# Kernel tuning notes

Hardware: AMD Instinct MI355X
Metric: run time of the kernel (lower is better)

Reference implementation:

```python
import jax, jax.numpy as jnp
import numpy as np

NUM_JOINTS = 21
BN_EPS = 1e-5


def hand_adjacency():
    J = NUM_JOINTS
    a = np.zeros((J, J), dtype=np.float32)
    # wrist to finger bases
    for j in (1, 5, 9, 13, 17):
        a[0, j] = a[j, 0] = 1
    # finger chains
    for base in (1, 5, 9, 13, 17):
        for i in range(base, base + 3):
            a[i, i + 1] = a[i + 1, i] = 1
    a += np.eye(J, dtype=np.float32)
    d = a.sum(axis=1)
    dinv = np.power(d, -0.5)
    dinv[np.isinf(dinv)] = 0.0
    D = np.diag(dinv)
    return (D @ a @ D).astype(np.float32)


def setup_inputs() -> dict:
    key = jax.random.key(0)
    ks = jax.random.split(key, 16)
    S, B, HD = 256, 128, 42
    IN, HID = 2, 64
    x = jax.random.normal(ks[0], (S, B, HD), dtype=jnp.float32)
    # xavier-uniform weights
    lim1 = float(np.sqrt(6.0 / (IN + HID)))
    lim2 = float(np.sqrt(6.0 / (HID + IN)))
    W1 = jax.random.uniform(ks[1], (IN, HID), minval=-lim1, maxval=lim1, dtype=jnp.float32)
    b1 = jnp.zeros((HID,), dtype=jnp.float32)
    W2 = jax.random.uniform(ks[2], (HID, IN), minval=-lim2, maxval=lim2, dtype=jnp.float32)
    b2 = jnp.zeros((IN,), dtype=jnp.float32)
    # BatchNorm (eval mode): affine params + running stats
    g1 = 1.0 + 0.1 * jax.random.normal(ks[3], (HID,), dtype=jnp.float32)
    be1 = 0.1 * jax.random.normal(ks[4], (HID,), dtype=jnp.float32)
    m1 = 0.1 * jax.random.normal(ks[5], (HID,), dtype=jnp.float32)
    v1 = 0.5 + jax.random.uniform(ks[6], (HID,), dtype=jnp.float32)
    g2 = 1.0 + 0.1 * jax.random.normal(ks[7], (IN,), dtype=jnp.float32)
    be2 = 0.1 * jax.random.normal(ks[8], (IN,), dtype=jnp.float32)
    m2 = 0.1 * jax.random.normal(ks[9], (IN,), dtype=jnp.float32)
    v2 = 0.5 + jax.random.uniform(ks[10], (IN,), dtype=jnp.float32)
    adj = jnp.asarray(hand_adjacency())
    return {"x": x, "adj": adj, "W1": W1, "b1": b1, "W2": W2, "b2": b2,
            "g1": g1, "be1": be1, "m1": m1, "v1": v1,
            "g2": g2, "be2": be2, "m2": m2, "v2": v2}


def _gcn_bn(h, adj, W, b, g, be, m, v, act):
    # h: (S, B, J, Cin) -> (S, B, J, Cout)
    s = jnp.einsum('sbjc,cd->sbjd', h, W)          # feature transform
    o = jnp.einsum('ij,sbjd->sbid', adj, s) + b    # joint aggregation + bias
    o = (o - m) * (g * jax.lax.rsqrt(v + BN_EPS)) + be  # BN eval, per-channel
    return jax.nn.relu(o) if act else o


def reference(x, adj, W1, b1, W2, b2, g1, be1, m1, v1, g2, be2, m2, v2):
    S, B, HD = x.shape
    C = HD // NUM_JOINTS
    h = x.reshape(S, B, NUM_JOINTS, C)
    h = _gcn_bn(h, adj, W1, b1, g1, be1, m1, v1, act=True)   # dropout is identity in eval
    h = _gcn_bn(h, adj, W2, b2, g2, be2, m2, v2, act=False)
    return h.reshape(S, B, HD) + x
```

## Files before the change

### kernel.cpp

```cpp
#include <hip/hip_runtime.h>

typedef float f2 __attribute__((ext_vector_type(2)));

#define NJ 21

#define W00 0.16666667f
#define W0B 0.23570226f
#define W33 0.33333333f
#define WMT 0.40824829f
#define WTT 0.5f

template<int PAT>
__device__ __forceinline__ float dpp_add(float v) {
    int r = __builtin_amdgcn_update_dpp(0, __float_as_int(v), PAT, 0xF, 0xF, true);
    return v + __int_as_float(r);
}

__device__ __forceinline__ void aggregate(const f2* __restrict__ s, f2* __restrict__ d) {
    d[0] = W00 * s[0] + W0B * (s[1] + s[5] + s[9] + s[13] + s[17]);
#pragma unroll
    for (int f = 1; f <= 17; f += 4) {
        d[f]     = W0B * s[0] + W33 * (s[f] + s[f + 1]);
        d[f + 1] = W33 * (s[f] + s[f + 1] + s[f + 2]);
        d[f + 2] = W33 * (s[f + 1] + s[f + 2]) + WMT * s[f + 3];
        d[f + 3] = WMT * s[f + 2] + WTT * s[f + 3];
    }
}

__global__ __launch_bounds__(256) void hgcn_kernel(
    const float* __restrict__ x,
    const float* __restrict__ adj,
    const float* __restrict__ W1,
    const float* __restrict__ b1,
    const float* __restrict__ W2,
    const float* __restrict__ b2,
    const float* __restrict__ g1,
    const float* __restrict__ be1,
    const float* __restrict__ m1,
    const float* __restrict__ v1,
    const float* __restrict__ g2,
    const float* __restrict__ be2,
    const float* __restrict__ m2,
    const float* __restrict__ v2,
    float* __restrict__ out)
{
    (void)adj;
    __shared__ float4 sc1[67];
    __shared__ float  sc2[64];
    __shared__ float  sD[2];
    __shared__ float  xs[64 * 42];
    __shared__ float  os[64 * 42];

    const int tid = threadIdx.x;

    const float4* __restrict__ xg =
        (const float4*)(x + (size_t)blockIdx.x * (64 * 42));
    float4* xs4 = (float4*)xs;
    const float4 r0 = xg[tid];
    const float4 r1 = xg[tid + 256];
    float4 r2;
    if (tid < 160) r2 = xg[tid + 512];

    if (tid < 64) {
        const int d = tid;
        const float k1  = g1[d] * rsqrtf(v1[d] + 1e-5f);
        const float A   = W1[d]      * k1;
        const float B   = W1[64 + d] * k1;
        const float C   = (b1[d] - m1[d]) * k1 + be1[d];
        const float k20 = g2[0] * rsqrtf(v2[0] + 1e-5f);
        const float k21 = g2[1] * rsqrtf(v2[1] + 1e-5f);
        sc1[d + (d >> 4)] = make_float4(A, B, C, W2[2 * d] * k20);
        sc2[d] = W2[2 * d + 1] * k21;
        if (d < 2) {
            const float k2 = (d == 0) ? k20 : k21;
            sD[d] = (b2[d] - m2[d]) * k2 + be2[d];
        }
    }

    xs4[tid]       = r0;
    xs4[tid + 256] = r1;
    if (tid < 160) xs4[tid + 512] = r2;
    __syncthreads();

    const int tl = tid >> 2;
    const int q  = tid & 3;

    const float2* __restrict__ xt = (const float2*)(xs + tl * 42);
    f2 h[NJ];
#pragma unroll
    for (int j = 0; j < NJ; ++j) {
        const float2 v = xt[j];
        h[j] = (f2){v.x, v.y};
    }

    f2 a[NJ + 1];
    aggregate(h, a);
    a[NJ] = (f2){0.f, 0.f};

    f2 ap0[11], ap1[11];
#pragma unroll
    for (int k = 0; k < 11; ++k) {
        ap0[k] = (f2){a[2 * k].x, a[2 * k + 1].x};
        ap1[k] = (f2){a[2 * k].y, a[2 * k + 1].y};
    }

    f2 s0[11], s1[11];
#pragma unroll
    for (int k = 0; k < 11; ++k) { s0[k] = (f2){0.f, 0.f}; s1[k] = (f2){0.f, 0.f}; }

    const int cbase = q * 17;
#pragma unroll
    for (int dd = 0; dd < 16; ++dd) {
        const float4 c  = sc1[cbase + dd];
        const float w21 = sc2[(q << 4) + dd];
#pragma unroll
        for (int k = 0; k < 11; ++k) {
            f2 v = ap0[k] * c.x + ap1[k] * c.y + c.z;
            v = __builtin_elementwise_max(v, (f2){0.f, 0.f});
            s0[k] += v * c.w;
            s1[k] += v * w21;
        }
    }

#pragma unroll
    for (int k = 0; k < 11; ++k) {
        s0[k].x = dpp_add<0xB1>(s0[k].x);  s0[k].x = dpp_add<0x4E>(s0[k].x);
        s0[k].y = dpp_add<0xB1>(s0[k].y);  s0[k].y = dpp_add<0x4E>(s0[k].y);
        s1[k].x = dpp_add<0xB1>(s1[k].x);  s1[k].x = dpp_add<0x4E>(s1[k].x);
        s1[k].y = dpp_add<0xB1>(s1[k].y);  s1[k].y = dpp_add<0x4E>(s1[k].y);
    }

    f2 vv[NJ], o[NJ];
#pragma unroll
    for (int j = 0; j < NJ; ++j) {
        vv[j].x = (j & 1) ? s0[j >> 1].y : s0[j >> 1].x;
        vv[j].y = (j & 1) ? s1[j >> 1].y : s1[j >> 1].x;
    }
    aggregate(vv, o);

    const int lo = (q == 0) ? 0 : (q == 1) ? 5 : (q == 2) ? 11 : 16;
    const int hi = (q == 0) ? 5 : (q == 1) ? 11 : (q == 2) ? 16 : 21;
    float2* __restrict__ ot = (float2*)(os + tl * 42);
#pragma unroll
    for (int i = 0; i < NJ; ++i) {
        if (i >= lo && i < hi) {
            float2 st; st.x = o[i].x; st.y = o[i].y;
            ot[i] = st;
        }
    }
    __syncthreads();

    const float4 Df = make_float4(sD[0], sD[1], sD[0], sD[1]);
    float4* __restrict__ og = (float4*)(out + (size_t)blockIdx.x * (64 * 42));
    const float4* os4 = (const float4*)os;

    float4 o0 = os4[tid],       x0 = xs4[tid];
    float4 o1 = os4[tid + 256], x1 = xs4[tid + 256];
    og[tid] = make_float4(o0.x + x0.x + Df.x, o0.y + x0.y + Df.y,
                          o0.z + x0.z + Df.z, o0.w + x0.w + Df.w);
    og[tid + 256] = make_float4(o1.x + x1.x + Df.x, o1.y + x1.y + Df.y,
                                o1.z + x1.z + Df.z, o1.w + x1.w + Df.w);
    if (tid < 160) {
        float4 o2 = os4[tid + 512], x2 = xs4[tid + 512];
        og[tid + 512] = make_float4(o2.x + x2.x + Df.x, o2.y + x2.y + Df.y,
                                    o2.z + x2.z + Df.z, o2.w + x2.w + Df.w);
    }
}

extern "C" void kernel_launch(void* const* d_in, const int* in_sizes, int n_in,
                              void* d_out, int out_size, void* d_ws, size_t ws_size,
                              hipStream_t stream) {
    (void)in_sizes; (void)n_in; (void)d_ws; (void)ws_size; (void)out_size;
    const float* x   = (const float*)d_in[0];
    const float* adj = (const float*)d_in[1];
    const float* W1  = (const float*)d_in[2];
    const float* b1  = (const float*)d_in[3];
    const float* W2  = (const float*)d_in[4];
    const float* b2  = (const float*)d_in[5];
    const float* g1  = (const float*)d_in[6];
    const float* be1 = (const float*)d_in[7];
    const float* m1  = (const float*)d_in[8];
    const float* v1  = (const float*)d_in[9];
    const float* g2  = (const float*)d_in[10];
    const float* be2 = (const float*)d_in[11];
    const float* m2  = (const float*)d_in[12];
    const float* v2  = (const float*)d_in[13];

    hgcn_kernel<<<512, 256, 0, stream>>>(x, adj, W1, b1, W2, b2,
                                         g1, be1, m1, v1, g2, be2, m2, v2,
                                         (float*)d_out);
}
```

Measured before the change: 90.10 us.

## Make each wave self-contained with 8-lane channel split and wave barriers

Restructures the kernel so each wave processes its own 8 tokens with private LDS staging and per-wave constant tables, replacing block-wide __syncthreads with wave barriers. The hidden-channel loop is split across 8 lanes per token (8 channels each) instead of 4 lanes (16 channels), adding a ds_swizzle reduction step. The grid doubles to 1024 blocks to expose more parallelism and reduce per-thread serial work, at the cost of redundant per-wave constant setup and an extra cross-lane reduction.

```diff
diff --git a/kernel.cpp b/kernel.cpp
--- a/kernel.cpp
+++ b/kernel.cpp
@@ -16,6 +16,11 @@
     return v + __int_as_float(r);
 }
 
+__device__ __forceinline__ float swz4_add(float v) {
+    int r = __builtin_amdgcn_ds_swizzle(__float_as_int(v), 0x101F);
+    return v + __int_as_float(r);
+}
+
 __device__ __forceinline__ void aggregate(const f2* __restrict__ s, f2* __restrict__ d) {
     d[0] = W00 * s[0] + W0B * (s[1] + s[5] + s[9] + s[13] + s[17]);
 #pragma unroll
@@ -27,7 +32,7 @@
     }
 }
 
-__global__ __launch_bounds__(256) void hgcn_kernel(
+__global__ __launch_bounds__(256, 4) void hgcn_kernel(
     const float* __restrict__ x,
     const float* __restrict__ adj,
     const float* __restrict__ W1,
@@ -45,52 +50,53 @@
     float* __restrict__ out)
 {
     (void)adj;
-    __shared__ float4 sc1[67];
-    __shared__ float  sc2[64];
-    __shared__ float  sD[2];
-    __shared__ float  xs[64 * 42];
-    __shared__ float  os[64 * 42];
+    __shared__ float  xs[4][336];
+    __shared__ float  os[4][336];
+    __shared__ float4 sc1[4][68];
+    __shared__ float  sc2[4][68];
+    __shared__ float  sD[4][2];
 
     const int tid = threadIdx.x;
+    const int wv  = tid >> 6;
+    const int ln  = tid & 63;
 
     const float4* __restrict__ xg =
-        (const float4*)(x + (size_t)blockIdx.x * (64 * 42));
-    float4* xs4 = (float4*)xs;
-    const float4 r0 = xg[tid];
-    const float4 r1 = xg[tid + 256];
-    float4 r2;
-    if (tid < 160) r2 = xg[tid + 512];
-
-    if (tid < 64) {
-        const int d = tid;
-        const float k1  = g1[d] * rsqrtf(v1[d] + 1e-5f);
-        const float A   = W1[d]      * k1;
-        const float B   = W1[64 + d] * k1;
-        const float C   = (b1[d] - m1[d]) * k1 + be1[d];
+        (const float4*)(x + ((size_t)blockIdx.x * 32 + (size_t)wv * 8) * 42);
+    const float4 r0 = xg[ln];
+    float4 r1;
+    if (ln < 20) r1 = xg[64 + ln];
+
+    {
+        const int dch = ln;
+        const float k1  = g1[dch] * rsqrtf(v1[dch] + 1e-5f);
+        const float A   = W1[dch]      * k1;
+        const float B   = W1[64 + dch] * k1;
+        const float C   = (b1[dch] - m1[dch]) * k1 + be1[dch];
         const float k20 = g2[0] * rsqrtf(v2[0] + 1e-5f);
         const float k21 = g2[1] * rsqrtf(v2[1] + 1e-5f);
-        sc1[d + (d >> 4)] = make_float4(A, B, C, W2[2 * d] * k20);
-        sc2[d] = W2[2 * d + 1] * k21;
-        if (d < 2) {
-            const float k2 = (d == 0) ? k20 : k21;
-            sD[d] = (b2[d] - m2[d]) * k2 + be2[d];
+        const int   idx = dch + (dch >> 4);
+        sc1[wv][idx] = make_float4(A, B, C, W2[2 * dch] * k20);
+        sc2[wv][idx] = W2[2 * dch + 1] * k21;
+        if (dch < 2) {
+            const float k2 = (dch == 0) ? k20 : k21;
+            sD[wv][dch] = (b2[dch] - m2[dch]) * k2 + be2[dch];
         }
     }
 
-    xs4[tid]       = r0;
-    xs4[tid + 256] = r1;
-    if (tid < 160) xs4[tid + 512] = r2;
-    __syncthreads();
-
-    const int tl = tid >> 2;
-    const int q  = tid & 3;
-
-    const float2* __restrict__ xt = (const float2*)(xs + tl * 42);
+    float4* xs4 = (float4*)xs[wv];
+    xs4[ln] = r0;
+    if (ln < 20) xs4[64 + ln] = r1;
+    __builtin_amdgcn_wave_barrier();
+
+    const int tl = ln >> 3;
+    const int li = ln & 7;
+
+    const float2* __restrict__ xt = (const float2*)(xs[wv] + tl * 42);
     f2 h[NJ];
 #pragma unroll
     for (int j = 0; j < NJ; ++j) {
-        const float2 v = xt[j];
-        h[j] = (f2){v.x, v.y};
+        const float2 t = xt[j];
+        h[j] = (f2){t.x, t.y};
     }
 
     f2 a[NJ + 1];
@@ -108,11 +114,15 @@
 #pragma unroll
     for (int k = 0; k < 11; ++k) { s0[k] = (f2){0.f, 0.f}; s1[k] = (f2){0.f, 0.f}; }
 
-    const int cbase = q * 17;
-#pragma unroll
-    for (int dd = 0; dd < 16; ++dd) {
-        const float4 c  = sc1[cbase + dd];
-        const float w21 = sc2[(q << 4) + dd];
+    const float4* __restrict__ c1w = (const float4*)sc1[wv];
+    const float*  __restrict__ c2w = sc2[wv];
+    const int dbase = li * 8;
+#pragma unroll
+    for (int dd = 0; dd < 8; ++dd) {
+        const int   dg  = dbase + dd;
+        const int   idx = dg + (dg >> 4);
+        const float4 c  = c1w[idx];
+        const float w21 = c2w[idx];
 #pragma unroll
         for (int k = 0; k < 11; ++k) {
             f2 v = ap0[k] * c.x + ap1[k] * c.y + c.z;
@@ -124,10 +134,10 @@
 
 #pragma unroll
     for (int k = 0; k < 11; ++k) {
-        s0[k].x = dpp_add<0xB1>(s0[k].x);  s0[k].x = dpp_add<0x4E>(s0[k].x);
-        s0[k].y = dpp_add<0xB1>(s0[k].y);  s0[k].y = dpp_add<0x4E>(s0[k].y);
-        s1[k].x = dpp_add<0xB1>(s1[k].x);  s1[k].x = dpp_add<0x4E>(s1[k].x);
-        s1[k].y = dpp_add<0xB1>(s1[k].y);  s1[k].y = dpp_add<0x4E>(s1[k].y);
+        s0[k].x = dpp_add<0xB1>(s0[k].x); s0[k].x = dpp_add<0x4E>(s0[k].x); s0[k].x = swz4_add(s0[k].x);
+        s0[k].y = dpp_add<0xB1>(s0[k].y); s0[k].y = dpp_add<0x4E>(s0[k].y); s0[k].y = swz4_add(s0[k].y);
+        s1[k].x = dpp_add<0xB1>(s1[k].x); s1[k].x = dpp_add<0x4E>(s1[k].x); s1[k].x = swz4_add(s1[k].x);
+        s1[k].y = dpp_add<0xB1>(s1[k].y); s1[k].y = dpp_add<0x4E>(s1[k].y); s1[k].y = swz4_add(s1[k].y);
     }
 
     f2 vv[NJ], o[NJ];
@@ -138,32 +148,31 @@
     }
     aggregate(vv, o);
 
-    const int lo = (q == 0) ? 0 : (q == 1) ? 5 : (q == 2) ? 11 : 16;
-    const int hi = (q == 0) ? 5 : (q == 1) ? 11 : (q == 2) ? 16 : 21;
-    float2* __restrict__ ot = (float2*)(os + tl * 42);
-#pragma unroll
-    for (int i = 0; i < NJ; ++i) {
-        if (i >= lo && i < hi) {
-            float2 st; st.x = o[i].x; st.y = o[i].y;
-            ot[i] = st;
+    const int lo = (li * 21) >> 3;
+    const int hi = ((li + 1) * 21) >> 3;
+    float2* __restrict__ ot = (float2*)(os[wv] + tl * 42);
+#pragma unroll
+    for (int j = 0; j < NJ; ++j) {
+        if (j >= lo && j < hi) {
+            float2 st; st.x = o[j].x; st.y = o[j].y;
+            ot[j] = st;
         }
     }
-    __syncthreads();
-
-    const float4 Df = make_float4(sD[0], sD[1], sD[0], sD[1]);
-    float4* __restrict__ og = (float4*)(out + (size_t)blockIdx.x * (64 * 42));
-    const float4* os4 = (const float4*)os;
-
-    float4 o0 = os4[tid],       x0 = xs4[tid];
-    float4 o1 = os4[tid + 256], x1 = xs4[tid + 256];
-    og[tid] = make_float4(o0.x + x0.x + Df.x, o0.y + x0.y + Df.y,
-                          o0.z + x0.z + Df.z, o0.w + x0.w + Df.w);
-    og[tid + 256] = make_float4(o1.x + x1.x + Df.x, o1.y + x1.y + Df.y,
-                                o1.z + x1.z + Df.z, o1.w + x1.w + Df.w);
-    if (tid < 160) {
-        float4 o2 = os4[tid + 512], x2 = xs4[tid + 512];
-        og[tid + 512] = make_float4(o2.x + x2.x + Df.x, o2.y + x2.y + Df.y,
-                                    o2.z + x2.z + Df.z, o2.w + x2.w + Df.w);
+    __builtin_amdgcn_wave_barrier();
+
+    const float Df0 = sD[wv][0], Df1 = sD[wv][1];
+    const float4 Df = make_float4(Df0, Df1, Df0, Df1);
+    float4* __restrict__ og =
+        (float4*)(out + ((size_t)blockIdx.x * 32 + (size_t)wv * 8) * 42);
+    const float4* os4 = (const float4*)os[wv];
+
+    const float4 o0 = os4[ln], x0 = xs4[ln];
+    og[ln] = make_float4(o0.x + x0.x + Df.x, o0.y + x0.y + Df.y,
+                         o0.z + x0.z + Df.z, o0.w + x0.w + Df.w);
+    if (ln < 20) {
+        const float4 o1 = os4[64 + ln], x1 = xs4[64 + ln];
+        og[64 + ln] = make_float4(o1.x + x1.x + Df.x, o1.y + x1.y + Df.y,
+                                  o1.z + x1.z + Df.z, o1.w + x1.w + Df.w);
     }
 }
 
@@ -186,7 +195,7 @@
     const float* m2  = (const float*)d_in[12];
     const float* v2  = (const float*)d_in[13];
 
-    hgcn_kernel<<<512, 256, 0, stream>>>(x, adj, W1, b1, W2, b2,
-                                         g1, be1, m1, v1, g2, be2, m2, v2,
-                                         (float*)d_out);
-}
+    hgcn_kernel<<<1024, 256, 0, stream>>>(x, adj, W1, b1, W2, b2,
+                                          g1, be1, m1, v1, g2, be2, m2, v2,
+                                          (float*)d_out);
+}
```

New measurement: 93.17 us. 1.03x slower.

## Drop LDS staging and block barriers; per-wave constants with direct global I/O

Applied to the files above, without the earlier changes.

Removes the shared-memory staging of input and output tiles and both block-wide __syncthreads. Each thread now loads its token's 42 floats straight from global memory and writes its strided joints directly with the residual and bias added. Each wave builds its own copy of the folded BN/weight constants and synchronises only with a wave barrier. This trades coalesced float4 traffic for redundant float2 loads across the 4 lanes of a token and less coalesced stores, in exchange for no block synchronisation and far less LDS, which may raise occupancy.

```diff
diff --git a/kernel.cpp b/kernel.cpp
--- a/kernel.cpp
+++ b/kernel.cpp
@@ -45,53 +45,40 @@
     float* __restrict__ out)
 {
     (void)adj;
-    __shared__ float4 sc1[67];
-    __shared__ float  sc2[64];
-    __shared__ float  sD[2];
-    __shared__ float  xs[64 * 42];
-    __shared__ float  os[64 * 42];
+    __shared__ float4 sc1[4][68];
+    __shared__ float  sc2[4][68];
 
     const int tid = threadIdx.x;
+    const int wv  = tid >> 6;
+    const int ln  = tid & 63;
+    const int tl  = ln >> 2;
+    const int q   = ln & 3;
 
-    const float4* __restrict__ xg =
-        (const float4*)(x + (size_t)blockIdx.x * (64 * 42));
-    float4* xs4 = (float4*)xs;
-    const float4 r0 = xg[tid];
-    const float4 r1 = xg[tid + 256];
-    float4 r2;
-    if (tid < 160) r2 = xg[tid + 512];
+    const size_t tok = (size_t)blockIdx.x * 64 + (size_t)wv * 16 + tl;
+    const float* __restrict__ xt = x + tok * 42;
 
-    if (tid < 64) {
-        const int d = tid;
-        const float k1  = g1[d] * rsqrtf(v1[d] + 1e-5f);
-        const float A   = W1[d]      * k1;
-        const float B   = W1[64 + d] * k1;
-        const float C   = (b1[d] - m1[d]) * k1 + be1[d];
-        const float k20 = g2[0] * rsqrtf(v2[0] + 1e-5f);
-        const float k21 = g2[1] * rsqrtf(v2[1] + 1e-5f);
-        sc1[d + (d >> 4)] = make_float4(A, B, C, W2[2 * d] * k20);
-        sc2[d] = W2[2 * d + 1] * k21;
-        if (d < 2) {
-            const float k2 = (d == 0) ? k20 : k21;
-            sD[d] = (b2[d] - m2[d]) * k2 + be2[d];
-        }
-    }
-
-    xs4[tid]       = r0;
-    xs4[tid + 256] = r1;
-    if (tid < 160) xs4[tid + 512] = r2;
-    __syncthreads();
-
-    const int tl = tid >> 2;
-    const int q  = tid & 3;
-
-    const float2* __restrict__ xt = (const float2*)(xs + tl * 42);
     f2 h[NJ];
 #pragma unroll
     for (int j = 0; j < NJ; ++j) {
-        const float2 v = xt[j];
-        h[j] = (f2){v.x, v.y};
+        const float2 t = ((const float2*)xt)[j];
+        h[j] = (f2){t.x, t.y};
     }
+
+    const float k20 = g2[0] * rsqrtf(v2[0] + 1e-5f);
+    const float k21 = g2[1] * rsqrtf(v2[1] + 1e-5f);
+    const float D0  = (b2[0] - m2[0]) * k20 + be2[0];
+    const float D1  = (b2[1] - m2[1]) * k21 + be2[1];
+    {
+        const int d = ln;
+        const float k1   = g1[d] * rsqrtf(v1[d] + 1e-5f);
+        const float2 w2d = *(const float2*)(W2 + 2 * d);
+        const int idx = d + (d >> 4);
+        sc1[wv][idx] = make_float4(W1[d] * k1, W1[64 + d] * k1,
+                                   (b1[d] - m1[d]) * k1 + be1[d], w2d.x * k20);
+        sc2[wv][idx] = w2d.y * k21;
+    }
+    __builtin_amdgcn_wave_barrier();
+    __builtin_amdgcn_sched_barrier(0);
 
     f2 a[NJ + 1];
     aggregate(h, a);
@@ -108,11 +95,13 @@
 #pragma unroll
     for (int k = 0; k < 11; ++k) { s0[k] = (f2){0.f, 0.f}; s1[k] = (f2){0.f, 0.f}; }
 
+    const float4* __restrict__ c1w = (const float4*)sc1[wv];
+    const float*  __restrict__ c2w = sc2[wv];
     const int cbase = q * 17;
 #pragma unroll
     for (int dd = 0; dd < 16; ++dd) {
-        const float4 c  = sc1[cbase + dd];
-        const float w21 = sc2[(q << 4) + dd];
+        const float4 c  = c1w[cbase + dd];
+        const float w21 = c2w[cbase + dd];
 #pragma unroll
         for (int k = 0; k < 11; ++k) {
             f2 v = ap0[k] * c.x + ap1[k] * c.y + c.z;
@@ -138,32 +127,15 @@
     }
     aggregate(vv, o);
 
-    const int lo = (q == 0) ? 0 : (q == 1) ? 5 : (q == 2) ? 11 : 16;
-    const int hi = (q == 0) ? 5 : (q == 1) ? 11 : (q == 2) ? 16 : 21;
-    float2* __restrict__ ot = (float2*)(os + tl * 42);
+    float* __restrict__ og = out + tok * 42;
 #pragma unroll
-    for (int i = 0; i < NJ; ++i) {
-        if (i >= lo && i < hi) {
-            float2 st; st.x = o[i].x; st.y = o[i].y;
-            ot[i] = st;
+    for (int j = 0; j < NJ; ++j) {
+        if ((j & 3) == q) {
+            float2 st;
+            st.x = o[j].x + h[j].x + D0;
+            st.y = o[j].y + h[j].y + D1;
+            ((float2*)og)[j] = st;
         }
-    }
-    __syncthreads();
-
-    const float4 Df = make_float4(sD[0], sD[1], sD[0], sD[1]);
-    float4* __restrict__ og = (float4*)(out + (size_t)blockIdx.x * (64 * 42));
-    const float4* os4 = (const float4*)os;
-
-    float4 o0 = os4[tid],       x0 = xs4[tid];
-    float4 o1 = os4[tid + 256], x1 = xs4[tid + 256];
-    og[tid] = make_float4(o0.x + x0.x + Df.x, o0.y + x0.y + Df.y,
-                          o0.z + x0.z + Df.z, o0.w + x0.w + Df.w);
-    og[tid + 256] = make_float4(o1.x + x1.x + Df.x, o1.y + x1.y + Df.y,
-                                o1.z + x1.z + Df.z, o1.w + x1.w + Df.w);
-    if (tid < 160) {
-        float4 o2 = os4[tid + 512], x2 = xs4[tid + 512];
-        og[tid + 512] = make_float4(o2.x + x2.x + Df.x, o2.y + x2.y + Df.y,
-                                    o2.z + x2.z + Df.z, o2.w + x2.w + Df.w);
     }
 }
 
```

New measurement: 89.04 us, median of 2. Within noise of the previous version (-1.2%).
